# Optimization experiments

Measured on AMD Instinct MI355X. Metric: run time of the kernel, lower is better.

The kernel has to match this reference:

```python
import jax, jax.numpy as jnp
import numpy as np

B1, B2 = 4096, 4096
DF, MF = 1024, 512
H1, H2, H3, H1_ = 2048, 1024, 512, 1024
DO, MO = 1, 1


def _lin(x, W, b):
    return x @ W.T + b


def setup_inputs() -> dict:
    key = jax.random.key(0)
    ks = jax.random.split(key, 22)

    def w(k, o, i):
        return (jax.random.normal(k, (o, i), jnp.float32) / np.sqrt(i)).astype(jnp.float32)

    def bz(k, o):
        return jax.random.normal(k, (o,), jnp.float32) * 0.01

    return {
        'x1': jax.random.normal(ks[0], (B1, DF), jnp.float32),
        'x2': jax.random.normal(ks[1], (B2, MF), jnp.float32),
        'W1_1': w(ks[2], H1, DF),  'b1_1': bz(ks[3], H1),
        'W1_2': w(ks[4], H2, H1),  'b1_2': bz(ks[5], H2),
        'W1_3': w(ks[6], H3, H2),  'b1_3': bz(ks[7], H3),
        'W1_4': w(ks[8], H2, H3),  'b1_4': bz(ks[9], H2),
        'W1_5': w(ks[10], H1, H2), 'b1_5': bz(ks[11], H1),
        'Wp1':  w(ks[12], DO, H1), 'bp1':  bz(ks[13], DO),
        'W2_1': w(ks[14], H1_, MF), 'b2_1': bz(ks[15], H1_),
        'W2_2': w(ks[16], H3, H1_), 'b2_2': bz(ks[17], H3),
        'W2_3': w(ks[18], H1_, H3), 'b2_3': bz(ks[19], H1_),
        'Wp2':  w(ks[20], MO, H1_), 'bp2':  bz(ks[21], MO),
    }


def reference(x1, x2, W1_1, b1_1, W1_2, b1_2, W1_3, b1_3, W1_4, b1_4,
              W1_5, b1_5, Wp1, bp1, W2_1, b2_1, W2_2, b2_2, W2_3, b2_3,
              Wp2, bp2):
    # dropout: eval mode (identity)
    h = jax.nn.relu(_lin(x1, W1_1, b1_1))
    h = jax.nn.relu(_lin(h, W1_2, b1_2))
    x_1 = jax.nn.sigmoid(_lin(h, W1_3, b1_3))          # [B1, H3]
    h = jax.nn.relu(_lin(x_1, W1_4, b1_4))
    h = jax.nn.relu(_lin(h, W1_5, b1_5))
    x2_1 = jax.nn.sigmoid(_lin(h, Wp1, bp1))           # [B1, DO]

    g = jax.nn.relu(_lin(x2, W2_1, b2_1))
    x_2 = jax.nn.sigmoid(_lin(g, W2_2, b2_2))          # [B2, H3]
    g = jax.nn.relu(_lin(x_2, W2_3, b2_3))
    x2_2 = jax.nn.sigmoid(_lin(g, Wp2, bp2))           # [B2, MO]

    # Python loop over x_1 rows doing (x_2 * row).sum(1) == single GEMM x_1 @ x_2.T
    scores = x_1 @ x_2.T                                # [B1, B2]
    pre_dm = scores.reshape(-1)                         # row-major matches torch.cat order
    # MinMaxScaler.fit_transform on detached values (original uses .data -> no grad)
    pre_dm = jax.lax.stop_gradient(pre_dm)
    mn, mx = pre_dm.min(), pre_dm.max()
    pre_dm = (pre_dm - mn) / (mx - mn)

    pre_data = x2_1.reshape(-1)
    pre_model = x2_2.T.reshape(-1)
    return (pre_data, pre_dm, pre_model)
```

## Files before the change

kernel.cpp:

```cpp
#include <hip/hip_runtime.h>
#include <hip/hip_bf16.h>

typedef __bf16 bf16_t;
typedef bf16_t bf16x8 __attribute__((ext_vector_type(8)));
typedef bf16_t bf16x4 __attribute__((ext_vector_type(4)));
typedef float f32x4 __attribute__((ext_vector_type(4)));

typedef __attribute__((address_space(1))) const void gconst_void;
typedef __attribute__((address_space(3))) void lds_void;

__device__ __forceinline__ void async16(const bf16_t* g, bf16_t* l) {
  __builtin_amdgcn_global_load_lds((gconst_void*)g, (lds_void*)l, 16, 0, 0);
}

struct CvtDesc { const float* src; bf16_t* dst; long n; };
struct CvtArgs { CvtDesc d[10]; };

__global__ __launch_bounds__(256) void cvt_many(CvtArgs a) {
  const CvtDesc de = a.d[blockIdx.y];
  long i = ((long)blockIdx.x * 256 + threadIdx.x) * 4;
  const long stride = (long)gridDim.x * 256 * 4;
  for (; i < de.n; i += stride) {
    float4 v = *(const float4*)(de.src + i);
    bf16x4 o;
    o[0] = (bf16_t)v.x; o[1] = (bf16_t)v.y; o[2] = (bf16_t)v.z; o[3] = (bf16_t)v.w;
    *(bf16x4*)(de.dst + i) = o;
  }
}

struct GDesc {
  const bf16_t* A; const bf16_t* W; const float* bias; void* C;
  int N, K, act;
};
struct GArgs { GDesc d[2]; int ntiles0; };

template <typename OutT, bool MINMAX>
__global__ __launch_bounds__(256) void gemm_gb(GArgs ga, float* __restrict__ pmin,
                                               float* __restrict__ pmax) {
  const int b = blockIdx.x;
  const int p = (b >= ga.ntiles0) ? 1 : 0;
  const GDesc d = ga.d[p];
  const int local = b - (p ? ga.ntiles0 : 0);
  const int bm = (local & 31) * 128;
  const int bn = (local >> 5) * 64;
  const int N = d.N, K = d.K;

  __shared__ __align__(16) bf16_t As[2][128 * 32];
  __shared__ __align__(16) bf16_t Bs[2][64 * 32];

  const int t = threadIdx.x;
  const int wave = t >> 6;
  const int lane = t & 63;
  const int quad = lane >> 4;
  const int l15 = lane & 15;
  const int wm = (wave >> 1) * 64;
  const int wn = (wave & 1) * 32;

  f32x4 acc[4][2];
#pragma unroll
  for (int i = 0; i < 4; ++i)
#pragma unroll
    for (int j = 0; j < 2; ++j) acc[i][j] = (f32x4){0.f, 0.f, 0.f, 0.f};

  const int c0 = t, c1 = t + 256;
  const int r0 = c0 >> 2, kc0 = ((c0 & 3) - r0 - (r0 >> 2)) & 3;
  const int r1 = c1 >> 2, kc1 = ((c1 & 3) - r1 - (r1 >> 2)) & 3;
  const bf16_t* pa0 = d.A + (long)(bm + r0) * K + kc0 * 8;
  const bf16_t* pa1 = d.A + (long)(bm + r1) * K + kc1 * 8;
  const bf16_t* pw0 = d.W + (long)(bn + r0) * K + kc0 * 8;
  bf16_t* lA0 = &As[0][c0 * 8]; bf16_t* lA1 = &As[0][c1 * 8];
  bf16_t* lB0 = &Bs[0][c0 * 8];
  const int bufOffA = 128 * 32;
  const int bufOffB = 64 * 32;

  async16(pa0, lA0); async16(pa1, lA1);
  async16(pw0, lB0);

  int buf = 0;
  for (int k0 = 0; k0 < K; k0 += 32) {
    __syncthreads();
    const int kn = k0 + 32;
    if (kn < K) {
      const int oA = (buf ^ 1) * bufOffA;
      const int oB = (buf ^ 1) * bufOffB;
      async16(pa0 + kn, lA0 + oA); async16(pa1 + kn, lA1 + oA);
      async16(pw0 + kn, lB0 + oB);
    }
    const bf16_t* as = As[buf];
    const bf16_t* bs = Bs[buf];
    bf16x8 af[4], bfr[2];
#pragma unroll
    for (int i = 0; i < 4; ++i) {
      const int r = wm + i * 16 + l15;
      af[i] = *(const bf16x8*)&as[r * 32 + ((quad + r + (r >> 2)) & 3) * 8];
    }
#pragma unroll
    for (int j = 0; j < 2; ++j) {
      const int r = wn + j * 16 + l15;
      bfr[j] = *(const bf16x8*)&bs[r * 32 + ((quad + r + (r >> 2)) & 3) * 8];
    }
#pragma unroll
    for (int i = 0; i < 4; ++i)
#pragma unroll
      for (int j = 0; j < 2; ++j)
        acc[i][j] = __builtin_amdgcn_mfma_f32_16x16x32_bf16(bfr[j], af[i],
                                                            acc[i][j], 0, 0, 0);
    buf ^= 1;
  }

  OutT* C = (OutT*)d.C;
  const int row0 = bm + wm + l15;
  const int col0 = bn + wn + quad * 4;
  float mn = 3.4e38f, mx = -3.4e38f;
#pragma unroll
  for (int i = 0; i < 4; ++i) {
    const long row = row0 + i * 16;
#pragma unroll
    for (int j = 0; j < 2; ++j) {
      const int col = col0 + j * 16;
      f32x4 bv = d.bias ? *(const f32x4*)&d.bias[col] : (f32x4){0.f, 0.f, 0.f, 0.f};
      f32x4 v;
#pragma unroll
      for (int r = 0; r < 4; ++r) {
        float x = acc[i][j][r] + bv[r];
        if (d.act == 1) x = fmaxf(x, 0.f);
        else if (d.act == 2) x = 1.f / (1.f + expf(-x));
        v[r] = x;
        if (MINMAX) { mn = fminf(mn, x); mx = fmaxf(mx, x); }
      }
      if constexpr (sizeof(OutT) == 4) {
        *(f32x4*)&((float*)C)[row * N + col] = v;
      } else {
        bf16x4 o;
        o[0] = (bf16_t)v[0]; o[1] = (bf16_t)v[1];
        o[2] = (bf16_t)v[2]; o[3] = (bf16_t)v[3];
        *(bf16x4*)&((bf16_t*)C)[row * N + col] = o;
      }
    }
  }
  if (MINMAX) {
#pragma unroll
    for (int off = 32; off > 0; off >>= 1) {
      mn = fminf(mn, __shfl_down(mn, off));
      mx = fmaxf(mx, __shfl_down(mx, off));
    }
    __shared__ float smn[4], smx[4];
    if (lane == 0) { smn[wave] = mn; smx[wave] = mx; }
    __syncthreads();
    if (t == 0) {
      pmin[blockIdx.x] = fminf(fminf(smn[0], smn[1]), fminf(smn[2], smn[3]));
      pmax[blockIdx.x] = fmaxf(fmaxf(smx[0], smx[1]), fmaxf(smx[2], smx[3]));
    }
  }
}

struct RDesc { const bf16_t* A; const float* w; const float* b; float* out; int K; };

__global__ __launch_bounds__(64) void rowdot2(RDesc d0, RDesc d1) {
  const RDesc d = blockIdx.y ? d1 : d0;
  const int row = blockIdx.x;
  const int lane = threadIdx.x;
  const bf16_t* a = d.A + (long)row * d.K;
  float s = 0.f;
  for (int k = lane * 8; k < d.K; k += 64 * 8) {
    bf16x8 av = *(const bf16x8*)&a[k];
    float4 w0 = *(const float4*)&d.w[k];
    float4 w1 = *(const float4*)&d.w[k + 4];
    s += (float)av[0] * w0.x + (float)av[1] * w0.y +
         (float)av[2] * w0.z + (float)av[3] * w0.w +
         (float)av[4] * w1.x + (float)av[5] * w1.y +
         (float)av[6] * w1.z + (float)av[7] * w1.w;
  }
#pragma unroll
  for (int off = 32; off > 0; off >>= 1) s += __shfl_down(s, off);
  if (lane == 0) d.out[row] = 1.f / (1.f + expf(-(s + d.b[0])));
}

__global__ __launch_bounds__(256) void minmax_final(
    const float* __restrict__ pmin, const float* __restrict__ pmax, int nb,
    float* __restrict__ res) {
  float mn = 3.4e38f, mx = -3.4e38f;
  for (int i = threadIdx.x; i < nb; i += 256) {
    mn = fminf(mn, pmin[i]);
    mx = fmaxf(mx, pmax[i]);
  }
#pragma unroll
  for (int off = 32; off > 0; off >>= 1) {
    mn = fminf(mn, __shfl_down(mn, off));
    mx = fmaxf(mx, __shfl_down(mx, off));
  }
  __shared__ float smn[4], smx[4];
  const int wv = threadIdx.x >> 6, ln = threadIdx.x & 63;
  if (ln == 0) { smn[wv] = mn; smx[wv] = mx; }
  __syncthreads();
  if (threadIdx.x == 0) {
    float m0 = fminf(fminf(smn[0], smn[1]), fminf(smn[2], smn[3]));
    float m1 = fmaxf(fmaxf(smx[0], smx[1]), fmaxf(smx[2], smx[3]));
    res[0] = m0;
    res[1] = 1.f / (m1 - m0);
  }
}

__global__ __launch_bounds__(256) void normalize_k(
    float* __restrict__ out, const float* __restrict__ res, long n) {
  const float mn = res[0], inv = res[1];
  long i = ((long)blockIdx.x * 256 + threadIdx.x) * 4;
  const long stride = (long)gridDim.x * 256 * 4;
  for (; i < n; i += stride) {
    float4 v = *(const float4*)&out[i];
    v.x = (v.x - mn) * inv;
    v.y = (v.y - mn) * inv;
    v.z = (v.z - mn) * inv;
    v.w = (v.w - mn) * inv;
    *(float4*)&out[i] = v;
  }
}

extern "C" void kernel_launch(void* const* d_in, const int* in_sizes, int n_in,
                              void* d_out, int out_size, void* d_ws,
                              size_t ws_size, hipStream_t stream) {
  const float* x1   = (const float*)d_in[0];
  const float* x2   = (const float*)d_in[1];
  const float* W1_1 = (const float*)d_in[2];   const float* b1_1 = (const float*)d_in[3];
  const float* W1_2 = (const float*)d_in[4];   const float* b1_2 = (const float*)d_in[5];
  const float* W1_3 = (const float*)d_in[6];   const float* b1_3 = (const float*)d_in[7];
  const float* W1_4 = (const float*)d_in[8];   const float* b1_4 = (const float*)d_in[9];
  const float* W1_5 = (const float*)d_in[10];  const float* b1_5 = (const float*)d_in[11];
  const float* Wp1  = (const float*)d_in[12];  const float* bp1  = (const float*)d_in[13];
  const float* W2_1 = (const float*)d_in[14];  const float* b2_1 = (const float*)d_in[15];
  const float* W2_2 = (const float*)d_in[16];  const float* b2_2 = (const float*)d_in[17];
  const float* W2_3 = (const float*)d_in[18];  const float* b2_3 = (const float*)d_in[19];
  const float* Wp2  = (const float*)d_in[20];  const float* bp2  = (const float*)d_in[21];

  float* out = (float*)d_out;
  float* out_pre_data  = out;
  float* out_pre_dm    = out + 4096;
  float* out_pre_model = out + 4096 + (long)4096 * 4096;

  char* arena = (char*)out_pre_dm;
  const size_t MB = 1024 * 1024;
  bf16_t* x1b   = (bf16_t*)(arena);
  bf16_t* x2b   = (bf16_t*)(arena + 8 * MB);
  bf16_t* W1_1b = (bf16_t*)(arena + 12 * MB);
  bf16_t* W1_2b = (bf16_t*)(arena + 16 * MB);
  bf16_t* W1_3b = (bf16_t*)(arena + 20 * MB);
  bf16_t* W1_4b = (bf16_t*)(arena + 21 * MB);
  bf16_t* W1_5b = (bf16_t*)(arena + 22 * MB);
  bf16_t* W2_1b = (bf16_t*)(arena + 26 * MB);
  bf16_t* W2_2b = (bf16_t*)(arena + 27 * MB);
  bf16_t* W2_3b = (bf16_t*)(arena + 28 * MB);
  bf16_t* bufA  = (bf16_t*)(arena + 32 * MB);
  bf16_t* bufB  = (bf16_t*)(arena + 48 * MB);
  bf16_t* bufC  = (bf16_t*)(arena + 56 * MB);

  char* ws = (char*)d_ws;
  bf16_t* bufX1 = (bf16_t*)(ws);
  bf16_t* bufX2 = (bf16_t*)(ws + 4 * MB);
  float* pmin = (float*)(ws + 8 * MB);
  float* pmax = pmin + 2048;
  float* res  = pmax + 2048;

  CvtArgs ca;
  ca.d[0] = {x1,   x1b,   (long)4096 * 1024};
  ca.d[1] = {x2,   x2b,   (long)4096 * 512};
  ca.d[2] = {W1_1, W1_1b, (long)2048 * 1024};
  ca.d[3] = {W1_2, W1_2b, (long)1024 * 2048};
  ca.d[4] = {W1_3, W1_3b, (long)512 * 1024};
  ca.d[5] = {W1_4, W1_4b, (long)1024 * 512};
  ca.d[6] = {W1_5, W1_5b, (long)2048 * 1024};
  ca.d[7] = {W2_1, W2_1b, (long)1024 * 512};
  ca.d[8] = {W2_2, W2_2b, (long)512 * 1024};
  ca.d[9] = {W2_3, W2_3b, (long)1024 * 512};
  cvt_many<<<dim3(192, 10), 256, 0, stream>>>(ca);

  const long nS = (long)4096 * 4096;
  GArgs g;

  g.d[0] = {x1b, W1_1b, b1_1, bufA, 2048, 1024, 1};
  g.d[1] = {x2b, W2_1b, b2_1, bufC, 1024, 512, 1};
  g.ntiles0 = 1024;
  gemm_gb<bf16_t, false><<<1536, 256, 0, stream>>>(g, nullptr, nullptr);

  g.d[0] = {bufA, W1_2b, b1_2, bufB, 1024, 2048, 1};
  g.d[1] = {bufC, W2_2b, b2_2, bufX2, 512, 1024, 2};
  g.ntiles0 = 512;
  gemm_gb<bf16_t, false><<<768, 256, 0, stream>>>(g, nullptr, nullptr);

  g.d[0] = {bufB, W1_3b, b1_3, bufX1, 512, 1024, 2};
  g.d[1] = {bufX2, W2_3b, b2_3, bufC, 1024, 512, 1};
  g.ntiles0 = 256;
  gemm_gb<bf16_t, false><<<768, 256, 0, stream>>>(g, nullptr, nullptr);

  g.d[0] = {bufX1, W1_4b, b1_4, bufB, 1024, 512, 1};
  g.d[1] = g.d[0];
  g.ntiles0 = 512;
  gemm_gb<bf16_t, false><<<512, 256, 0, stream>>>(g, nullptr, nullptr);

  g.d[0] = {bufB, W1_5b, b1_5, bufA, 2048, 1024, 1};
  g.d[1] = g.d[0];
  g.ntiles0 = 1024;
  gemm_gb<bf16_t, false><<<1024, 256, 0, stream>>>(g, nullptr, nullptr);

  RDesc r0 = {bufA, Wp1, bp1, out_pre_data, 2048};
  RDesc r1 = {bufC, Wp2, bp2, out_pre_model, 1024};
  rowdot2<<<dim3(4096, 2), 64, 0, stream>>>(r0, r1);

  g.d[0] = {bufX1, bufX2, nullptr, out_pre_dm, 4096, 512, 0};
  g.d[1] = g.d[0];
  g.ntiles0 = 2048;
  gemm_gb<float, true><<<2048, 256, 0, stream>>>(g, pmin, pmax);

  minmax_final<<<1, 256, 0, stream>>>(pmin, pmax, 2048, res);
  normalize_k<<<2048, 256, 0, stream>>>(out_pre_dm, res, nS);
}
```

Measured before the change: 358.6 us.

## Triple-buffer GEMM LDS tiles with explicit vmcnt waits and raw barriers

Changes the GEMM main loop from double to triple buffering of the A and W tiles in LDS. Loads run two k-steps ahead, and synchronisation uses explicit s_waitcnt vmcnt counts plus raw s_barrier instead of __syncthreads, so memory latency overlaps more with MFMA work. The cost is 50% more LDS per block, which may lower occupancy. Correctness now depends on the hand-counted vmcnt values and on K being at least 64.

```diff
diff --git a/kernel.cpp b/kernel.cpp
--- a/kernel.cpp
+++ b/kernel.cpp
@@ -45,8 +45,8 @@
   const int bn = (local >> 5) * 64;
   const int N = d.N, K = d.K;
 
-  __shared__ __align__(16) bf16_t As[2][128 * 32];
-  __shared__ __align__(16) bf16_t Bs[2][64 * 32];
+  __shared__ __align__(16) bf16_t As[3][128 * 32];
+  __shared__ __align__(16) bf16_t Bs[3][64 * 32];
 
   const int t = threadIdx.x;
   const int wave = t >> 6;
@@ -73,21 +73,16 @@
   const int bufOffA = 128 * 32;
   const int bufOffB = 64 * 32;
 
-  async16(pa0, lA0); async16(pa1, lA1);
-  async16(pw0, lB0);
-
-  int buf = 0;
-  for (int k0 = 0; k0 < K; k0 += 32) {
-    __syncthreads();
-    const int kn = k0 + 32;
-    if (kn < K) {
-      const int oA = (buf ^ 1) * bufOffA;
-      const int oB = (buf ^ 1) * bufOffB;
-      async16(pa0 + kn, lA0 + oA); async16(pa1 + kn, lA1 + oA);
-      async16(pw0 + kn, lB0 + oB);
-    }
-    const bf16_t* as = As[buf];
-    const bf16_t* bs = Bs[buf];
+  auto stage = [&](int ke, int bi) {
+    const int oA = bi * bufOffA, oB = bi * bufOffB;
+    async16(pa0 + ke, lA0 + oA);
+    async16(pa1 + ke, lA1 + oA);
+    async16(pw0 + ke, lB0 + oB);
+  };
+
+  auto compute = [&](int bi) {
+    const bf16_t* as = As[bi];
+    const bf16_t* bs = Bs[bi];
     bf16x8 af[4], bfr[2];
 #pragma unroll
     for (int i = 0; i < 4; ++i) {
@@ -100,13 +95,37 @@
       bfr[j] = *(const bf16x8*)&bs[r * 32 + ((quad + r + (r >> 2)) & 3) * 8];
     }
 #pragma unroll
-    for (int i = 0; i < 4; ++i)
-#pragma unroll
-      for (int j = 0; j < 2; ++j)
-        acc[i][j] = __builtin_amdgcn_mfma_f32_16x16x32_bf16(bfr[j], af[i],
-                                                            acc[i][j], 0, 0, 0);
-    buf ^= 1;
-  }
+    for (int i = 0; i < 4; ++i) {
+      acc[i][0] = __builtin_amdgcn_mfma_f32_16x16x32_bf16(bfr[0], af[i],
+                                                          acc[i][0], 0, 0, 0);
+      acc[i][1] = __builtin_amdgcn_mfma_f32_16x16x32_bf16(bfr[1], af[i],
+                                                          acc[i][1], 0, 0, 0);
+    }
+  };
+
+  const int nsteps = K >> 5;
+  stage(0, 0);
+  stage(32, 1);
+  int s = 0;
+  for (; s < nsteps - 2; ++s) {
+    __builtin_amdgcn_s_barrier();
+    __builtin_amdgcn_sched_barrier(0);
+    stage((s + 2) * 32, (s + 2) % 3);
+    asm volatile("s_waitcnt vmcnt(6)" ::: "memory");
+    __builtin_amdgcn_s_barrier();
+    __builtin_amdgcn_sched_barrier(0);
+    compute(s % 3);
+  }
+  __builtin_amdgcn_s_barrier();
+  asm volatile("s_waitcnt vmcnt(3)" ::: "memory");
+  __builtin_amdgcn_s_barrier();
+  __builtin_amdgcn_sched_barrier(0);
+  compute(s % 3);
+  ++s;
+  asm volatile("s_waitcnt vmcnt(0)" ::: "memory");
+  __builtin_amdgcn_s_barrier();
+  __builtin_amdgcn_sched_barrier(0);
+  compute(s % 3);
 
   OutT* C = (OutT*)d.C;
   const int row0 = bm + wm + l15;
```

Result: no change. 357.8 us (-0.2%).
